# Kernel optimization log

Hardware: AMD Instinct MI355X
Metric: run time of the kernel (lower is better)

The kernel has to match this reference:

```python
import jax, jax.numpy as jnp
import numpy as np

N = 100000   # nodes
E = 1600000  # edges (avg degree 16)
F_IN, H1, H2, H3, C = 500, 200, 100, 40, 3


def setup_inputs() -> dict:
    key = jax.random.key(0)
    ks = jax.random.split(key, 10)
    def w(k, shape, fan_in):
        return jax.random.normal(k, shape, dtype=jnp.float32) / np.sqrt(fan_in)
    return {
        "x": jax.random.normal(ks[0], (N, F_IN), dtype=jnp.float32),
        "edge_index": jax.random.randint(ks[1], (2, E), 0, N, dtype=jnp.int32),
        "W1": w(ks[2], (H1, F_IN), F_IN), "b1": jnp.zeros((H1,), jnp.float32),
        "W1b": w(ks[3], (H2, H1), H1),  "b1b": jnp.zeros((H2,), jnp.float32),
        "W2b": w(ks[4], (H3, H2), H2),  "b2b": jnp.zeros((H3,), jnp.float32),
        "W2": w(ks[5], (C, H3), H3),    "b2": jnp.zeros((C,), jnp.float32),
    }


def _gcn_conv(x, W, b, src, dst, norm_e, n):
    # GCNConv: linear transform, then normalized scatter-add aggregation, then bias
    h = x @ W.T                                   # [N, out]
    msgs = h[src] * norm_e[:, None]               # [E+N, out] gathered, normalized
    out = jax.ops.segment_sum(msgs, dst, num_segments=n)
    return out + b


def reference(x, edge_index, W1, b1, W1b, b1b, W2b, b2b, W2, b2):
    n = x.shape[0]
    loop = jnp.arange(n, dtype=edge_index.dtype)
    src = jnp.concatenate([edge_index[0], loop])  # add self-loops (GCNConv default)
    dst = jnp.concatenate([edge_index[1], loop])
    # symmetric normalization: deg computed on target nodes, norm = d^-1/2[src]*d^-1/2[dst]
    deg = jax.ops.segment_sum(jnp.ones_like(dst, dtype=x.dtype), dst, num_segments=n)
    dinv = jnp.where(deg > 0, jax.lax.rsqrt(deg), 0.0)
    norm_e = dinv[src] * dinv[dst]

    # dropout(p=0.5, training=self.training) is identity at inference
    h = jax.nn.relu(_gcn_conv(x, W1, b1, src, dst, norm_e, n))
    h = jax.nn.relu(_gcn_conv(h, W1b, b1b, src, dst, norm_e, n))
    h = jax.nn.relu(_gcn_conv(h, W2b, b2b, src, dst, norm_e, n))
    return _gcn_conv(h, W2, b2, src, dst, norm_e, n)
```

## Files before the change

### kernel.cpp

```cpp
#include <hip/hip_runtime.h>


#define DEV __device__ __forceinline__

typedef __attribute__((ext_vector_type(8))) short short8;
typedef __attribute__((ext_vector_type(8))) _Float16 f16x8;
typedef __attribute__((ext_vector_type(4))) float f32x4;
typedef __attribute__((ext_vector_type(4))) _Float16 f16x4;

DEV void gload_lds16(const void* g, void* l) {
    __builtin_amdgcn_global_load_lds(
        (const __attribute__((address_space(1))) unsigned int*)g,
        (__attribute__((address_space(3))) unsigned int*)l, 16, 0, 0);
}


__global__ void k_init(int* __restrict__ cnt, int* __restrict__ fill, int n) {
    int i = blockIdx.x * 256 + threadIdx.x;
    if (i < n) { cnt[i] = 1; fill[i] = 0; }
}

__global__ void k_count(const int* __restrict__ dst, int* __restrict__ cnt, int E) {
    int e = blockIdx.x * 256 + threadIdx.x;
    if (e < E) atomicAdd(&cnt[dst[e]], 1);
}

__global__ void k_scan1(const int* __restrict__ cnt, int* __restrict__ row_start,
                        int* __restrict__ partial, float* __restrict__ dinv, int n) {
    __shared__ int sdata[256];
    int base = blockIdx.x * 1024;
    int t = threadIdx.x;
    int v[4]; int sum = 0;
#pragma unroll
    for (int j = 0; j < 4; ++j) {
        int idx = base + t * 4 + j;
        v[j] = (idx < n) ? cnt[idx] : 0;
        if (idx < n) dinv[idx] = rsqrtf((float)v[j]);
        sum += v[j];
    }
    sdata[t] = sum;
    __syncthreads();
    for (int off = 1; off < 256; off <<= 1) {
        int x = (t >= off) ? sdata[t - off] : 0;
        __syncthreads();
        sdata[t] += x;
        __syncthreads();
    }
    int excl = sdata[t] - sum;
#pragma unroll
    for (int j = 0; j < 4; ++j) {
        int idx = base + t * 4 + j;
        if (idx < n) row_start[idx] = excl;
        excl += v[j];
    }
    if (t == 255) partial[blockIdx.x] = sdata[255];
}

__global__ void k_scan2(int* __restrict__ partial, int nb) {
    __shared__ int s[128];
    int t = threadIdx.x;
    int v = (t < nb) ? partial[t] : 0;
    s[t] = v;
    __syncthreads();
    for (int off = 1; off < 128; off <<= 1) {
        int x = (t >= off) ? s[t - off] : 0;
        __syncthreads();
        s[t] += x;
        __syncthreads();
    }
    if (t < nb) partial[t] = s[t] - v;
}

__global__ void k_scan3(int* __restrict__ row_start, const int* __restrict__ partial,
                        int n, int total) {
    int i = blockIdx.x * 256 + threadIdx.x;
    if (i < n) row_start[i] += partial[i >> 10];
    if (i == 0) row_start[n] = total;
}

__global__ void k_fill(const int* __restrict__ src, const int* __restrict__ dst,
                       const int* __restrict__ row_start, int* __restrict__ fill,
                       int* __restrict__ csr_src, int E, int n) {
    int i = blockIdx.x * 256 + threadIdx.x;
    int total = E + n;
    if (i >= total) return;
    int s, d;
    if (i < E) { s = src[i]; d = dst[i]; }
    else       { s = d = i - E; }
    int pos = row_start[d] + atomicAdd(&fill[d], 1);
    csr_src[pos] = s;
}


__global__ void k_wcvt16(const float* __restrict__ W, int N, int K,
                         unsigned short* __restrict__ Wh, int NPAD, int KPAD) {
    int i = blockIdx.x * 256 + threadIdx.x;
    if (i >= NPAD * KPAD) return;
    int r = i / KPAD, k = i - r * KPAD;
    float x = (r < N && k < K) ? W[r * K + k] : 0.f;
    Wh[i] = __builtin_bit_cast(unsigned short, (_Float16)x);
}
__global__ void k_wdec16(const float* __restrict__ W, int N, int K,
                         unsigned short* __restrict__ Wh, unsigned short* __restrict__ Wl,
                         int NPAD, int KPAD) {
    int i = blockIdx.x * 256 + threadIdx.x;
    if (i >= NPAD * KPAD) return;
    int r = i / KPAD, k = i - r * KPAD;
    float x = (r < N && k < K) ? W[r * K + k] : 0.f;
    _Float16 h = (_Float16)x;
    _Float16 l = (_Float16)((x - (float)h) * 2048.0f);
    Wh[i] = __builtin_bit_cast(unsigned short, h);
    Wl[i] = __builtin_bit_cast(unsigned short, l);
}


struct A8 { f32x4 lo, hi; };

template <int NFC, int KP, int HILO, int MODE, typename AT>
__global__ __launch_bounds__(512, 2)
void gemm_res(const AT* __restrict__ A, int lda, int M, int K,
              const unsigned short* __restrict__ Wh,
              const unsigned short* __restrict__ Wl,
              const float* __restrict__ dinv,
              _Float16* __restrict__ H16, int ldh, int Nout) {
    constexpr int NPAD = NFC * 16;
    constexpr int CHH  = NPAD * KP / 8;
    constexpr int CHT  = CHH * (1 + HILO);
    constexpr int NIT  = (CHT + 511) / 512;
    constexpr int SB   = NPAD * 64;
    constexpr int HB   = CHH * 16;
    constexpr int NS   = KP / 32;
    __shared__ char lds[CHT * 16];

    const int tid  = threadIdx.x;
    const int wv   = tid >> 6;
    const int lane = tid & 63;
    const int lr   = lane & 15;
    const int kq   = lane >> 4;
    const int m0   = blockIdx.x * 256;
    const int col0 = blockIdx.y * NPAD;

    const unsigned short* WhB = Wh + (size_t)col0 * KP;
    const unsigned short* WlB = Wl + (size_t)col0 * KP;

#pragma unroll
    for (int i = 0; i < NIT; ++i) {
        int c = tid + i * 512;
        if ((CHT % 512 == 0) || (c < CHT)) {
            int h  = (HILO && c >= CHH) ? 1 : 0;
            int cc = c - h * CHH;
            int s  = cc / (NPAD * 4);
            int rm = cc - s * (NPAD * 4);
            int r  = rm >> 2;
            int sl = rm & 3;
            int gs = sl ^ (r & 3);
            const unsigned short* gp = (h ? WlB : WhB) + (size_t)r * KP + s * 32 + gs * 8;
            gload_lds16(gp, lds + (size_t)c * 16);
        }
    }

    int arow0 = m0 + wv * 32 + lr;       if (arow0 >= M) arow0 = M - 1;
    int arow1 = m0 + wv * 32 + 16 + lr;  if (arow1 >= M) arow1 = M - 1;
    const AT* Arow0 = A + (size_t)arow0 * lda;
    const AT* Arow1 = A + (size_t)arow1 * lda;

    auto loadA32 = [&](const AT* Arow, int s) -> A8 {
        A8 o;
        int kb = s * 32 + kq * 8;
        if (kb + 8 <= K) {
            const float* ap = (const float*)Arow + kb;
            o.lo = *(const f32x4*)ap;
            o.hi = *(const f32x4*)(ap + 4);
        } else {
#pragma unroll
            for (int i = 0; i < 4; ++i) {
                int k0 = kb + i, k1 = kb + 4 + i;
                o.lo[i] = (k0 < K) ? (float)Arow[k0] : 0.f;
                o.hi[i] = (k1 < K) ? (float)Arow[k1] : 0.f;
            }
        }
        return o;
    };
    auto loadA16 = [&](const AT* Arow, int s) -> short8 {
        int kb = s * 32 + kq * 8;
        if (kb + 8 <= K) return *(const short8*)((const unsigned short*)Arow + kb);
        short8 o;
        const unsigned short* ap = (const unsigned short*)Arow;
#pragma unroll
        for (int i = 0; i < 8; ++i) o[i] = (kb + i < K) ? (short)ap[kb + i] : (short)0;
        return o;
    };
    auto cvtA = [&](const A8& a) -> f16x8 {
        f16x8 o;
#pragma unroll
        for (int i = 0; i < 4; ++i) {
            o[i]     = (_Float16)a.lo[i];
            o[4 + i] = (_Float16)a.hi[i];
        }
        return o;
    };

    f32x4 acP[NFC], acQ[NFC], alP[NFC], alQ[NFC];
#pragma unroll
    for (int f = 0; f < NFC; ++f) {
        acP[f] = (f32x4){0.f, 0.f, 0.f, 0.f};
        acQ[f] = (f32x4){0.f, 0.f, 0.f, 0.f};
        alP[f] = (f32x4){0.f, 0.f, 0.f, 0.f};
        alQ[f] = (f32x4){0.f, 0.f, 0.f, 0.f};
    }

    __syncthreads();

    const int ro = lr * 64 + ((kq ^ (lr & 3)) << 4);

#pragma unroll
    for (int s = 0; s < NS; ++s) {
        f16x8 a0, a1;
        if constexpr (MODE == 0) {
            a0 = cvtA(loadA32(Arow0, s));
            a1 = cvtA(loadA32(Arow1, s));
        } else {
            a0 = __builtin_bit_cast(f16x8, loadA16(Arow0, s));
            a1 = __builtin_bit_cast(f16x8, loadA16(Arow1, s));
        }
        const char* bb = lds + s * SB;
#pragma unroll
        for (int f = 0; f < NFC; ++f) {
            f16x8 bh = __builtin_bit_cast(f16x8, *(const short8*)(bb + f * 1024 + ro));
            acP[f] = __builtin_amdgcn_mfma_f32_16x16x32_f16(a0, bh, acP[f], 0, 0, 0);
            acQ[f] = __builtin_amdgcn_mfma_f32_16x16x32_f16(a1, bh, acQ[f], 0, 0, 0);
            if constexpr (HILO) {
                f16x8 bl = __builtin_bit_cast(f16x8, *(const short8*)(bb + HB + f * 1024 + ro));
                alP[f] = __builtin_amdgcn_mfma_f32_16x16x32_f16(a0, bl, alP[f], 0, 0, 0);
                alQ[f] = __builtin_amdgcn_mfma_f32_16x16x32_f16(a1, bl, alQ[f], 0, 0, 0);
            }
        }
    }

    {
        const int rbase = m0 + wv * 32 + kq * 4;
        float dv[4];
#pragma unroll
        for (int j = 0; j < 4; ++j) {
            int row = rbase + j;
            dv[j] = (row < M) ? dinv[row] : 0.f;
        }
#pragma unroll
        for (int f = 0; f < NFC; ++f) {
            int col = col0 + f * 16 + lr;
            if (col >= Nout) continue;
#pragma unroll
            for (int j = 0; j < 4; ++j) {
                int row = rbase + j;
                if (row >= M) continue;
                float v = acP[f][j];
                if constexpr (HILO) v += alP[f][j] * (1.0f / 2048.0f);
                H16[(size_t)row * ldh + col] = (_Float16)(v * dv[j]);
            }
        }
    }
    {
        const int rbase = m0 + wv * 32 + 16 + kq * 4;
        float dv[4];
#pragma unroll
        for (int j = 0; j < 4; ++j) {
            int row = rbase + j;
            dv[j] = (row < M) ? dinv[row] : 0.f;
        }
#pragma unroll
        for (int f = 0; f < NFC; ++f) {
            int col = col0 + f * 16 + lr;
            if (col >= Nout) continue;
#pragma unroll
            for (int j = 0; j < 4; ++j) {
                int row = rbase + j;
                if (row >= M) continue;
                float v = acQ[f][j];
                if constexpr (HILO) v += alQ[f][j] * (1.0f / 2048.0f);
                H16[(size_t)row * ldh + col] = (_Float16)(v * dv[j]);
            }
        }
    }
}


template <int F, bool RELU>
__global__ __launch_bounds__(256)
void agg_f16(const _Float16* __restrict__ h, const int* __restrict__ row_start,
             const int* __restrict__ csr_src, const float* __restrict__ dinv,
             const float* __restrict__ bias, _Float16* __restrict__ out, int n,
             int ldo) {
    constexpr int LPN = F / 4;
    constexpr int NPW = 64 / LPN;
    int wave = blockIdx.x * 4 + (threadIdx.x >> 6);
    int lane = threadIdx.x & 63;
    int sub  = lane / LPN;
    int fi   = lane - sub * LPN;
    int node = wave * NPW + sub;
    if (sub >= NPW || node >= n) return;
    int f = fi * 4;
    const _Float16* hf = h + f;

    f32x4 acc = {0.f, 0.f, 0.f, 0.f};
    int e0 = row_start[node], e1 = row_start[node + 1];
    int e = e0;
    for (; e + 4 <= e1; e += 4) {
        int s0 = csr_src[e + 0];
        int s1 = csr_src[e + 1];
        int s2 = csr_src[e + 2];
        int s3 = csr_src[e + 3];
        f16x4 v0 = *(const f16x4*)&hf[(size_t)s0 * F];
        f16x4 v1 = *(const f16x4*)&hf[(size_t)s1 * F];
        f16x4 v2 = *(const f16x4*)&hf[(size_t)s2 * F];
        f16x4 v3 = *(const f16x4*)&hf[(size_t)s3 * F];
        acc += __builtin_convertvector(v0, f32x4);
        acc += __builtin_convertvector(v1, f32x4);
        acc += __builtin_convertvector(v2, f32x4);
        acc += __builtin_convertvector(v3, f32x4);
    }
    for (; e < e1; ++e) {
        int s = csr_src[e];
        f16x4 v = *(const f16x4*)&hf[(size_t)s * F];
        acc += __builtin_convertvector(v, f32x4);
    }
    float dn = dinv[node];
    f32x4 b4 = *(const f32x4*)&bias[f];
    acc = acc * dn + b4;
    if (RELU) {
#pragma unroll
        for (int j = 0; j < 4; ++j) acc[j] = fmaxf(acc[j], 0.f);
    }
    f16x4 o;
#pragma unroll
    for (int j = 0; j < 4; ++j) o[j] = (_Float16)acc[j];
    *(f16x4*)&out[(size_t)node * ldo + f] = o;
}


__global__ void gemm_small(const _Float16* __restrict__ A, const float* __restrict__ B,
                           const float* __restrict__ dinv, float* __restrict__ C,
                           int M, int K) {
    int m = blockIdx.x * 256 + threadIdx.x;
    if (m >= M) return;
    float a0 = 0.f, a1 = 0.f, a2 = 0.f;
    for (int k = 0; k < K; ++k) {
        float a = (float)A[(size_t)m * K + k];
        a0 += a * B[0 * K + k];
        a1 += a * B[1 * K + k];
        a2 += a * B[2 * K + k];
    }
    float dv = dinv[m];
    C[(size_t)m * 3 + 0] = a0 * dv;
    C[(size_t)m * 3 + 1] = a1 * dv;
    C[(size_t)m * 3 + 2] = a2 * dv;
}

__global__ void agg_f3(const float* __restrict__ h, const int* __restrict__ row_start,
                       const int* __restrict__ csr_src, const float* __restrict__ dinv,
                       const float* __restrict__ bias, float* __restrict__ out, int n) {
    int i = blockIdx.x * 256 + threadIdx.x;
    if (i >= n * 3) return;
    int node = i / 3;
    int f = i - node * 3;
    float acc = 0.f;
    int e1 = row_start[node + 1];
    for (int e = row_start[node]; e < e1; ++e) {
        int s = csr_src[e];
        acc += h[(size_t)s * 3 + f];
    }
    out[i] = acc * dinv[node] + bias[f];
}


extern "C" void kernel_launch(void* const* d_in, const int* in_sizes, int n_in,
                              void* d_out, int out_size, void* d_ws, size_t ws_size,
                              hipStream_t stream) {
    const float* x   = (const float*)d_in[0];
    const int*   ei  = (const int*)d_in[1];
    const float* W1  = (const float*)d_in[2];
    const float* b1  = (const float*)d_in[3];
    const float* W1b = (const float*)d_in[4];
    const float* b1b = (const float*)d_in[5];
    const float* W2b = (const float*)d_in[6];
    const float* b2b = (const float*)d_in[7];
    const float* W2  = (const float*)d_in[8];
    const float* b2  = (const float*)d_in[9];
    float* out = (float*)d_out;

    const int F_IN = 500, H1 = 200, H2 = 100, H3 = 40;
    const int N = in_sizes[0] / F_IN;
    const int E = in_sizes[1] / 2;
    const int* src = ei;
    const int* dst = ei + E;

    size_t off = 0;
    auto alloc = [&](size_t bytes) -> void* {
        void* p = (char*)d_ws + off;
        off += (bytes + 255) & ~(size_t)255;
        return p;
    };
    int*   cnt       = (int*)  alloc((size_t)N * 4);
    int*   row_start = (int*)  alloc((size_t)(N + 1) * 4);
    int*   fill      = (int*)  alloc((size_t)N * 4);
    int*   partial   = (int*)  alloc(128 * 4);
    float* dinv      = (float*)alloc((size_t)N * 4);
    int*   csr_src   = (int*)  alloc((size_t)(E + N) * 4);
    unsigned short* wh1 = (unsigned short*)alloc(224 * 512 * 2);
    unsigned short* wh2 = (unsigned short*)alloc(112 * 224 * 2);
    unsigned short* wl2 = (unsigned short*)alloc(112 * 224 * 2);
    unsigned short* wh3 = (unsigned short*)alloc(48 * 128 * 2);
    unsigned short* wl3 = (unsigned short*)alloc(48 * 128 * 2);
    _Float16* h16   = (_Float16*)alloc((size_t)N * H1 * 2);
    _Float16* act16 = (_Float16*)alloc((size_t)N * H1 * 2);
    float*    bufC  = (float*)   alloc((size_t)N * 3 * 4);

    int gN  = (N + 255) / 256;
    int gE  = (E + 255) / 256;
    int gEN = (E + N + 255) / 256;
    int nb  = (N + 1023) / 1024;

    k_init <<<gN, 256, 0, stream>>>(cnt, fill, N);
    k_count<<<gE, 256, 0, stream>>>(dst, cnt, E);
    k_scan1<<<nb, 256, 0, stream>>>(cnt, row_start, partial, dinv, N);
    k_scan2<<<1, 128, 0, stream>>>(partial, nb);
    k_scan3<<<gN, 256, 0, stream>>>(row_start, partial, N, E + N);
    k_fill <<<gEN, 256, 0, stream>>>(src, dst, row_start, fill, csr_src, E, N);

    k_wcvt16<<<(224 * 512 + 255) / 256, 256, 0, stream>>>(W1,  H1, F_IN, wh1, 224, 512);
    k_wdec16<<<(112 * 224 + 255) / 256, 256, 0, stream>>>(W1b, H2, H1, wh2, wl2, 112, 224);
    k_wdec16<<<( 48 * 128 + 255) / 256, 256, 0, stream>>>(W2b, H3, H2, wh3, wl3,  48, 128);

    const int gM = (N + 255) / 256;

    gemm_res<7, 512, 0, 0, float><<<dim3(gM, 2), 512, 0, stream>>>(
        x, F_IN, N, F_IN, wh1, wh1, dinv, h16, H1, H1);
    agg_f16<200, true><<<(N + 3) / 4, 256, 0, stream>>>(h16, row_start, csr_src, dinv,
                                                        b1, act16, N, 200);
    gemm_res<7, 224, 1, 1, _Float16><<<dim3(gM, 1), 512, 0, stream>>>(
        act16, 200, N, H1, wh2, wl2, dinv, h16, H2, H2);
    agg_f16<100, true><<<(N / 2 + 3) / 4, 256, 0, stream>>>(h16, row_start, csr_src, dinv,
                                                            b1b, act16, N, 112);
    gemm_res<3, 128, 1, 1, _Float16><<<dim3(gM, 1), 512, 0, stream>>>(
        act16, 112, N, H2, wh3, wl3, dinv, h16, H3, H3);
    {
        int waves = (N + 5) / 6, blocks = (waves + 3) / 4;
        agg_f16<40, true><<<blocks, 256, 0, stream>>>(h16, row_start, csr_src, dinv,
                                                      b2b, act16, N, 40);
    }
    gemm_small<<<(N + 255) / 256, 256, 0, stream>>>(act16, W2, dinv, bufC, N, H3);
    agg_f3<<<(N * 3 + 255) / 256, 256, 0, stream>>>(bufC, row_start, csr_src, dinv,
                                                    b2, out, N);
}
```

Baseline: 568.0 us.

## Prefetch GEMM A-tiles into registers, swap grid axes, widen aggregation gathers to 8 halfs

The GEMM now keeps up to 8 k-slices of A in registers and loads each slice several iterations before it is used, which hides global-load latency behind the MFMAs. The grid axes are swapped so that column blocks sharing the same rows are scheduled next to each other, which improves L2 reuse of the A rows. The aggregation kernel gains a vector-width parameter: the 200- and 40-feature layers use 16-byte f16x8 gathers, so each wave covers more nodes per gather. The cost is higher register pressure from the prefetch buffers, especially for the float-input layer-1 GEMM, and this could lower occupancy.

```diff
diff --git a/kernel.cpp b/kernel.cpp
--- a/kernel.cpp
+++ b/kernel.cpp
@@ -100,6 +100,7 @@
     float x = (r < N && k < K) ? W[r * K + k] : 0.f;
     Wh[i] = __builtin_bit_cast(unsigned short, (_Float16)x);
 }
+
 __global__ void k_wdec16(const float* __restrict__ W, int N, int K,
                          unsigned short* __restrict__ Wh, unsigned short* __restrict__ Wl,
                          int NPAD, int KPAD) {
@@ -130,6 +131,7 @@
     constexpr int SB   = NPAD * 64;
     constexpr int HB   = CHH * 16;
     constexpr int NS   = KP / 32;
+    constexpr int D    = (NS < 8) ? NS : 8;
     __shared__ char lds[CHT * 16];
 
     const int tid  = threadIdx.x;
@@ -137,8 +139,8 @@
     const int lane = tid & 63;
     const int lr   = lane & 15;
     const int kq   = lane >> 4;
-    const int m0   = blockIdx.x * 256;
-    const int col0 = blockIdx.y * NPAD;
+    const int m0   = blockIdx.y * 256;
+    const int col0 = blockIdx.x * NPAD;
 
     const unsigned short* WhB = Wh + (size_t)col0 * KP;
     const unsigned short* WlB = Wl + (size_t)col0 * KP;
@@ -200,6 +202,16 @@
         return o;
     };
 
+    A8 ab0[D], ab1[D];
+    short8 hb0[D], hb1[D];
+#pragma unroll
+    for (int p = 0; p < D; ++p) {
+        if (p < NS) {
+            if constexpr (MODE == 0) { ab0[p] = loadA32(Arow0, p); ab1[p] = loadA32(Arow1, p); }
+            else                     { hb0[p] = loadA16(Arow0, p); hb1[p] = loadA16(Arow1, p); }
+        }
+    }
+
     f32x4 acP[NFC], acQ[NFC], alP[NFC], alQ[NFC];
 #pragma unroll
     for (int f = 0; f < NFC; ++f) {
@@ -216,13 +228,14 @@
 #pragma unroll
     for (int s = 0; s < NS; ++s) {
         f16x8 a0, a1;
-        if constexpr (MODE == 0) {
-            a0 = cvtA(loadA32(Arow0, s));
-            a1 = cvtA(loadA32(Arow1, s));
-        } else {
-            a0 = __builtin_bit_cast(f16x8, loadA16(Arow0, s));
-            a1 = __builtin_bit_cast(f16x8, loadA16(Arow1, s));
-        }
+        if constexpr (MODE == 0) { a0 = cvtA(ab0[s % D]); a1 = cvtA(ab1[s % D]); }
+        else { a0 = __builtin_bit_cast(f16x8, hb0[s % D]); a1 = __builtin_bit_cast(f16x8, hb1[s % D]); }
+
+        if (s + D < NS) {
+            if constexpr (MODE == 0) { ab0[s % D] = loadA32(Arow0, s + D); ab1[s % D] = loadA32(Arow1, s + D); }
+            else                     { hb0[s % D] = loadA16(Arow0, s + D); hb1[s % D] = loadA16(Arow1, s + D); }
+        }
+
         const char* bb = lds + s * SB;
 #pragma unroll
         for (int f = 0; f < NFC; ++f) {
@@ -284,13 +297,13 @@
 }
 
 
-template <int F, bool RELU>
+template <int F, int VEC, bool RELU>
 __global__ __launch_bounds__(256)
 void agg_f16(const _Float16* __restrict__ h, const int* __restrict__ row_start,
              const int* __restrict__ csr_src, const float* __restrict__ dinv,
              const float* __restrict__ bias, _Float16* __restrict__ out, int n,
              int ldo) {
-    constexpr int LPN = F / 4;
+    constexpr int LPN = F / VEC;
     constexpr int NPW = 64 / LPN;
     int wave = blockIdx.x * 4 + (threadIdx.x >> 6);
     int lane = threadIdx.x & 63;
@@ -298,10 +311,26 @@
     int fi   = lane - sub * LPN;
     int node = wave * NPW + sub;
     if (sub >= NPW || node >= n) return;
-    int f = fi * 4;
+    int f = fi * VEC;
     const _Float16* hf = h + f;
 
-    f32x4 acc = {0.f, 0.f, 0.f, 0.f};
+    f32x4 acc0 = {0.f, 0.f, 0.f, 0.f};
+    f32x4 acc1 = {0.f, 0.f, 0.f, 0.f};
+
+    auto addv = [&](const _Float16* p) {
+        if constexpr (VEC == 8) {
+            f16x8 v = *(const f16x8*)p;
+            f16x4 vl, vh;
+#pragma unroll
+            for (int j = 0; j < 4; ++j) { vl[j] = v[j]; vh[j] = v[4 + j]; }
+            acc0 += __builtin_convertvector(vl, f32x4);
+            acc1 += __builtin_convertvector(vh, f32x4);
+        } else {
+            f16x4 v = *(const f16x4*)p;
+            acc0 += __builtin_convertvector(v, f32x4);
+        }
+    };
+
     int e0 = row_start[node], e1 = row_start[node + 1];
     int e = e0;
     for (; e + 4 <= e1; e += 4) {
@@ -309,31 +338,40 @@
         int s1 = csr_src[e + 1];
         int s2 = csr_src[e + 2];
         int s3 = csr_src[e + 3];
-        f16x4 v0 = *(const f16x4*)&hf[(size_t)s0 * F];
-        f16x4 v1 = *(const f16x4*)&hf[(size_t)s1 * F];
-        f16x4 v2 = *(const f16x4*)&hf[(size_t)s2 * F];
-        f16x4 v3 = *(const f16x4*)&hf[(size_t)s3 * F];
-        acc += __builtin_convertvector(v0, f32x4);
-        acc += __builtin_convertvector(v1, f32x4);
-        acc += __builtin_convertvector(v2, f32x4);
-        acc += __builtin_convertvector(v3, f32x4);
-    }
-    for (; e < e1; ++e) {
-        int s = csr_src[e];
-        f16x4 v = *(const f16x4*)&hf[(size_t)s * F];
-        acc += __builtin_convertvector(v, f32x4);
-    }
+        const _Float16* p0 = &hf[(size_t)s0 * F];
+        const _Float16* p1 = &hf[(size_t)s1 * F];
+        const _Float16* p2 = &hf[(size_t)s2 * F];
+        const _Float16* p3 = &hf[(size_t)s3 * F];
+        addv(p0); addv(p1); addv(p2); addv(p3);
+    }
+    for (; e < e1; ++e) addv(&hf[(size_t)csr_src[e] * F]);
+
     float dn = dinv[node];
-    f32x4 b4 = *(const f32x4*)&bias[f];
-    acc = acc * dn + b4;
-    if (RELU) {
-#pragma unroll
-        for (int j = 0; j < 4; ++j) acc[j] = fmaxf(acc[j], 0.f);
-    }
-    f16x4 o;
-#pragma unroll
-    for (int j = 0; j < 4; ++j) o[j] = (_Float16)acc[j];
-    *(f16x4*)&out[(size_t)node * ldo + f] = o;
+    if constexpr (VEC == 8) {
+        f32x4 b0 = *(const f32x4*)&bias[f];
+        f32x4 b1 = *(const f32x4*)&bias[f + 4];
+        acc0 = acc0 * dn + b0;
+        acc1 = acc1 * dn + b1;
+        if (RELU) {
+#pragma unroll
+            for (int j = 0; j < 4; ++j) { acc0[j] = fmaxf(acc0[j], 0.f); acc1[j] = fmaxf(acc1[j], 0.f); }
+        }
+        f16x8 o;
+#pragma unroll
+        for (int j = 0; j < 4; ++j) { o[j] = (_Float16)acc0[j]; o[4 + j] = (_Float16)acc1[j]; }
+        *(f16x8*)&out[(size_t)node * ldo + f] = o;
+    } else {
+        f32x4 b4 = *(const f32x4*)&bias[f];
+        acc0 = acc0 * dn + b4;
+        if (RELU) {
+#pragma unroll
+            for (int j = 0; j < 4; ++j) acc0[j] = fmaxf(acc0[j], 0.f);
+        }
+        f16x4 o;
+#pragma unroll
+        for (int j = 0; j < 4; ++j) o[j] = (_Float16)acc0[j];
+        *(f16x4*)&out[(size_t)node * ldo + f] = o;
+    }
 }
 
 
@@ -432,20 +470,23 @@
 
     const int gM = (N + 255) / 256;
 
-    gemm_res<7, 512, 0, 0, float><<<dim3(gM, 2), 512, 0, stream>>>(
+    gemm_res<7, 512, 0, 0, float><<<dim3(2, gM), 512, 0, stream>>>(
         x, F_IN, N, F_IN, wh1, wh1, dinv, h16, H1, H1);
-    agg_f16<200, true><<<(N + 3) / 4, 256, 0, stream>>>(h16, row_start, csr_src, dinv,
-                                                        b1, act16, N, 200);
-    gemm_res<7, 224, 1, 1, _Float16><<<dim3(gM, 1), 512, 0, stream>>>(
+    {
+        int waves = (N + 1) / 2, blocks = (waves + 3) / 4;
+        agg_f16<200, 8, true><<<blocks, 256, 0, stream>>>(h16, row_start, csr_src, dinv,
+                                                          b1, act16, N, 200);
+    }
+    gemm_res<7, 224, 1, 1, _Float16><<<dim3(1, gM), 512, 0, stream>>>(
         act16, 200, N, H1, wh2, wl2, dinv, h16, H2, H2);
-    agg_f16<100, true><<<(N / 2 + 3) / 4, 256, 0, stream>>>(h16, row_start, csr_src, dinv,
-                                                            b1b, act16, N, 112);
-    gemm_res<3, 128, 1, 1, _Float16><<<dim3(gM, 1), 512, 0, stream>>>(
+    agg_f16<100, 4, true><<<(N / 2 + 3) / 4, 256, 0, stream>>>(h16, row_start, csr_src, dinv,
+                                                               b1b, act16, N, 112);
+    gemm_res<3, 128, 1, 1, _Float16><<<dim3(1, gM), 512, 0, stream>>>(
         act16, 112, N, H2, wh3, wl3, dinv, h16, H3, H3);
     {
-        int waves = (N + 5) / 6, blocks = (waves + 3) / 4;
-        agg_f16<40, true><<<blocks, 256, 0, stream>>>(h16, row_start, csr_src, dinv,
-                                                      b2b, act16, N, 40);
+        int waves = (N + 11) / 12, blocks = (waves + 3) / 4;
+        agg_f16<40, 8, true><<<blocks, 256, 0, stream>>>(h16, row_start, csr_src, dinv,
+                                                         b2b, act16, N, 40);
     }
     gemm_small<<<(N + 255) / 256, 256, 0, stream>>>(act16, W2, dinv, bufC, N, H3);
     agg_f3<<<(N * 3 + 255) / 256, 256, 0, stream>>>(bufC, row_start, csr_src, dinv,
```

Result: slower. 590.0 us (+3.9%).
